# Optimization experiments

Measured on AMD Instinct MI355X. Metric: run time of the kernel, lower is better.

The kernel has to match this reference:

```python
import jax, jax.numpy as jnp
import numpy as np

N_NODES = 100000
N_EDGES = 1600000
D = 128
LEAKY_SLOPE = 0.01  # torch nn.LeakyReLU default


def setup_inputs() -> dict:
    key = jax.random.key(0)
    k1, k2, k3, k4 = jax.random.split(key, 4)
    in_states = jax.random.normal(k1, (N_NODES, D), dtype=jnp.float32)
    edges = jax.random.randint(k2, (2, N_EDGES), 0, N_NODES, dtype=jnp.int64)
    # Linear weights, kaiming-uniform-ish scale
    W_msg = jax.random.normal(k3, (D, D), dtype=jnp.float32) / np.sqrt(D)
    attn_w = jax.random.normal(k4, (2 * D,), dtype=jnp.float32) / np.sqrt(2 * D)
    W_res = jnp.eye(D, dtype=jnp.float32)  # eye-initialized, frozen residual proj
    passthrough_coef = jnp.ones((1,), dtype=jnp.float32)
    return {"in_states": in_states, "edges": edges, "W_msg": W_msg,
            "attn_w": attn_w, "W_res": W_res, "passthrough_coef": passthrough_coef}


def reference(in_states, edges, W_msg, attn_w, W_res, passthrough_coef):
    n_nodes = in_states.shape[0]
    src, dst = edges[0], edges[1]

    # message transform (dropout in eval mode -> identity)
    messages = in_states @ W_msg.T                       # [N, D]

    # attention score: Linear(2D->1) on cat([m_from, m_to]) == split dot products
    s_from = messages @ attn_w[:D]                       # [N]
    s_to = messages @ attn_w[D:]                         # [N]
    e = s_from[src] + s_to[dst]                          # [E]
    e = jnp.where(e >= 0, e, LEAKY_SLOPE * e)            # LeakyReLU

    # indexed (segment) softmax over destination nodes
    seg_max = jax.ops.segment_max(e, dst, num_segments=n_nodes)
    e_exp = jnp.exp(e - seg_max[dst])
    seg_sum = jax.ops.segment_sum(e_exp, dst, num_segments=n_nodes)
    alpha = e_exp / seg_sum[dst]                         # [E]

    # weighted scatter-add aggregation
    scaled = alpha[:, None] * messages[src]              # [E, D]
    merged = jax.ops.segment_sum(scaled, dst, num_segments=n_nodes)  # [N, D]

    new_states_res = jax.nn.relu(merged)
    old_passthrough = (in_states @ W_res.T) * jax.nn.sigmoid(passthrough_coef[0])
    return old_passthrough + new_states_res
```

## Files before the change

kernel.cpp:

```cpp
#include <hip/hip_runtime.h>
#include <hip/hip_fp16.h>


#define DD 128
#define NPB 32
#define LEAKY 0.01f
#define BSH 3
#define BSZ 8

#define FMA4(A, XS, W)                                        \
  A.x = fmaf((XS), (W).x, A.x); A.y = fmaf((XS), (W).y, A.y); \
  A.z = fmaf((XS), (W).z, A.z); A.w = fmaf((XS), (W).w, A.w)

__global__ void k_init(const int* __restrict__ e, const float* __restrict__ Wr,
                       int* __restrict__ flag, int* __restrict__ bcnt, int nb) {
  const int b = blockIdx.x;
  if (b == 0) {
    if (threadIdx.x == 0) {
      int all0 = 1;
      for (int i = 0; i < 64; ++i)
        if (e[2 * i + 1] != 0) { all0 = 0; break; }
      flag[0] = all0;
    }
  } else if (b == 1) {
    __shared__ int ok_s;
    if (threadIdx.x == 0) ok_s = 1;
    __syncthreads();
    int ok = 1;
    for (int i = threadIdx.x; i < DD * DD; i += 256) {
      float expect = ((i >> 7) == (i & (DD - 1))) ? 1.f : 0.f;
      if (Wr[i] != expect) ok = 0;
    }
    if (!ok) ok_s = 0;
    __syncthreads();
    if (threadIdx.x == 0) flag[1] = ok_s;
  } else {
    int i = (b - 2) * 256 + threadIdx.x;
    if (i < nb) bcnt[i] = 0;
  }
}

__global__ void k_prep(const float* __restrict__ Wm, const float* __restrict__ Wr,
                       float* __restrict__ WTm, float* __restrict__ WTr,
                       const int* __restrict__ edges, int n_edges, int n_nodes,
                       const int* __restrict__ flag, int* __restrict__ bcnt) {
  const int b = blockIdx.x;
  if (b < 64) {
    int idx = b * 256 + threadIdx.x;
    int j = idx >> 7, k = idx & (DD - 1);
    WTm[k * DD + j] = Wm[idx];
    WTr[k * DD + j] = Wr[idx];
  } else {
    int i = (b - 64) * 256 + threadIdx.x;
    if (i < n_edges) {
      int d = flag[0] ? ((const int2*)edges)[n_edges + i].x : edges[n_edges + i];
      if ((unsigned)d < (unsigned)n_nodes) atomicAdd(&bcnt[d >> BSH], 1);
    }
  }
}

__global__ __launch_bounds__(256) void k_scan_a(const int* __restrict__ cnt, int n,
                                                int* __restrict__ outp,
                                                int* __restrict__ bsum) {
  __shared__ int lds[256];
  const int t = threadIdx.x;
  const int base = blockIdx.x * 1024 + t * 4;
  int v0 = 0, v1 = 0, v2 = 0, v3 = 0;
  if (base + 3 < n) {
    int4 q = *(const int4*)(cnt + base);
    v0 = q.x; v1 = q.y; v2 = q.z; v3 = q.w;
  } else {
    if (base + 0 < n) v0 = cnt[base + 0];
    if (base + 1 < n) v1 = cnt[base + 1];
    if (base + 2 < n) v2 = cnt[base + 2];
    if (base + 3 < n) v3 = cnt[base + 3];
  }
  const int tsum = v0 + v1 + v2 + v3;
  int val = tsum;
  lds[t] = val;
  __syncthreads();
  for (int off = 1; off < 256; off <<= 1) {
    int a = (t >= off) ? lds[t - off] : 0;
    __syncthreads();
    val += a;
    lds[t] = val;
    __syncthreads();
  }
  int o0 = val - tsum;
  int o1 = o0 + v0, o2 = o1 + v1, o3 = o2 + v2;
  if (base + 0 < n) outp[base + 0] = o0;
  if (base + 1 < n) outp[base + 1] = o1;
  if (base + 2 < n) outp[base + 2] = o2;
  if (base + 3 < n) outp[base + 3] = o3;
  if (t == 255) bsum[blockIdx.x] = val;
}

__global__ void k_scan_b(int* __restrict__ bsum, int nbk,
                         int* __restrict__ bstart, int nb) {
  __shared__ int lds[256];
  const int t = threadIdx.x;
  int v = (t < nbk) ? bsum[t] : 0;
  int val = v;
  lds[t] = val;
  __syncthreads();
  for (int off = 1; off < 256; off <<= 1) {
    int a = (t >= off) ? lds[t - off] : 0;
    __syncthreads();
    val += a;
    lds[t] = val;
    __syncthreads();
  }
  if (t < nbk) bsum[t] = val - v;
  if (t == nbk - 1) bstart[nb] = val;
}

__global__ void k_scan_c(int* __restrict__ bstart, int* __restrict__ bcursor,
                         const int* __restrict__ bsum, int nb) {
  const int off = bsum[blockIdx.x];
  const int base = blockIdx.x * 1024 + threadIdx.x * 4;
#pragma unroll
  for (int c = 0; c < 4; ++c) {
    int idx = base + c;
    if (idx < nb) {
      int r = bstart[idx] + off;
      bstart[idx] = r;
      bcursor[idx] = r;
    }
  }
}

__global__ __launch_bounds__(256) void k_mscat(
    const float* __restrict__ x, const float* __restrict__ WTm,
    const float* __restrict__ WTr, const float* __restrict__ attn_w,
    const float* __restrict__ coef, const int* __restrict__ flag, int n_nodes,
    __half* __restrict__ mh, float* __restrict__ s_from,
    float* __restrict__ s_to, float* __restrict__ out, int msg_blocks,
    const int* __restrict__ edges, int n_edges, int* __restrict__ bcursor,
    int* __restrict__ packed) {
  __shared__ float4 lw4[32 * 32];
  __shared__ float4 lx4[NPB * 32];
  __shared__ float lds_aw[2 * DD];
  const int t = threadIdx.x;

  if ((int)blockIdx.x >= msg_blocks) {
    int i = (blockIdx.x - msg_blocks) * 256 + t;
    if (i < n_edges) {
      int d, s;
      if (flag[0]) {
        d = ((const int2*)edges)[n_edges + i].x;
        s = ((const int2*)edges)[i].x;
      } else {
        d = edges[n_edges + i];
        s = edges[i];
      }
      if ((unsigned)d < (unsigned)n_nodes) {
        if ((unsigned)s >= (unsigned)n_nodes) s = 0;
        int pos = atomicAdd(&bcursor[d >> BSH], 1);
        packed[pos] = (s << BSH) | (d & (BSZ - 1));
      }
    }
    return;
  }

  const int base = blockIdx.x * NPB;
  const int nvalid = min(NPB, n_nodes - base);

  const float4* xs = (const float4*)(x + (size_t)base * DD);
  const int nflt4 = nvalid * 32;
  for (int i = t; i < nflt4; i += 256) lx4[i] = xs[i];
  if (t < 2 * DD) lds_aw[t] = attn_w[t];

  const int j4 = t & 31;
  const int g = t >> 5;
  const int r0 = (g * 4 + 0) * 32, r1 = r0 + 32, r2 = r1 + 32, r3 = r2 + 32;

  float4 a0, a1, a2, a3;

#define GEMM128(WT)                                                           \
  a0 = a1 = a2 = a3 = make_float4(0.f, 0.f, 0.f, 0.f);                        \
  _Pragma("unroll 1")                                                         \
  for (int chunk = 0; chunk < 4; ++chunk) {                                   \
    __syncthreads();                                                          \
    const float4* wsrc = (const float4*)((WT) + chunk * 32 * DD);             \
    lw4[t] = wsrc[t];                                                         \
    lw4[t + 256] = wsrc[t + 256];                                             \
    lw4[t + 512] = wsrc[t + 512];                                             \
    lw4[t + 768] = wsrc[t + 768];                                             \
    __syncthreads();                                                          \
    const int xb = chunk * 8;                                                 \
    _Pragma("unroll 2")                                                       \
    for (int k = 0; k < 32; k += 4) {                                         \
      float4 w0 = lw4[(k + 0) * 32 + j4];                                     \
      float4 w1 = lw4[(k + 1) * 32 + j4];                                     \
      float4 w2 = lw4[(k + 2) * 32 + j4];                                     \
      float4 w3 = lw4[(k + 3) * 32 + j4];                                     \
      float4 x0 = lx4[r0 + xb + (k >> 2)];                                    \
      float4 x1 = lx4[r1 + xb + (k >> 2)];                                    \
      float4 x2 = lx4[r2 + xb + (k >> 2)];                                    \
      float4 x3 = lx4[r3 + xb + (k >> 2)];                                    \
      FMA4(a0, x0.x, w0); FMA4(a0, x0.y, w1);                                 \
      FMA4(a0, x0.z, w2); FMA4(a0, x0.w, w3);                                 \
      FMA4(a1, x1.x, w0); FMA4(a1, x1.y, w1);                                 \
      FMA4(a1, x1.z, w2); FMA4(a1, x1.w, w3);                                 \
      FMA4(a2, x2.x, w0); FMA4(a2, x2.y, w1);                                 \
      FMA4(a2, x2.z, w2); FMA4(a2, x2.w, w3);                                 \
      FMA4(a3, x3.x, w0); FMA4(a3, x3.y, w1);                                 \
      FMA4(a3, x3.z, w2); FMA4(a3, x3.w, w3);                                 \
    }                                                                         \
  }

  GEMM128(WTm);
  {
    float4 av[4] = {a0, a1, a2, a3};
#pragma unroll
    for (int b = 0; b < 4; ++b) {
      int n = g * 4 + b;
      if (n < nvalid) {
        int gn = base + n;
        float4 v = av[b];
        union { __half2 h2[2]; uint2 u; } pk;
        pk.h2[0] = __floats2half2_rn(v.x, v.y);
        pk.h2[1] = __floats2half2_rn(v.z, v.w);
        ((uint2*)(mh + (size_t)gn * DD))[j4] = pk.u;
        float sf = v.x * lds_aw[4 * j4] + v.y * lds_aw[4 * j4 + 1] +
                   v.z * lds_aw[4 * j4 + 2] + v.w * lds_aw[4 * j4 + 3];
        float stv = v.x * lds_aw[DD + 4 * j4] + v.y * lds_aw[DD + 4 * j4 + 1] +
                    v.z * lds_aw[DD + 4 * j4 + 2] + v.w * lds_aw[DD + 4 * j4 + 3];
#pragma unroll
        for (int m = 16; m; m >>= 1) {
          sf += __shfl_xor(sf, m, 32);
          stv += __shfl_xor(stv, m, 32);
        }
        if (j4 == 0) { s_from[gn] = sf; s_to[gn] = stv; }
      }
    }
  }

  const float sig = 1.f / (1.f + __expf(-coef[0]));
  if (flag[1]) {
    float4* od = (float4*)(out + (size_t)base * DD);
    for (int i = t; i < nflt4; i += 256) {
      float4 v = lx4[i];
      v.x *= sig; v.y *= sig; v.z *= sig; v.w *= sig;
      od[i] = v;
    }
  } else {
    GEMM128(WTr);
    float4 av[4] = {a0, a1, a2, a3};
#pragma unroll
    for (int b = 0; b < 4; ++b) {
      int n = g * 4 + b;
      if (n < nvalid) {
        int gn = base + n;
        float4 v = av[b];
        v.x *= sig; v.y *= sig; v.z *= sig; v.w *= sig;
        ((float4*)(out + (size_t)gn * DD))[j4] = v;
      }
    }
  }
#undef GEMM128
}

__global__ __launch_bounds__(256) void k_bsort(
    const int* __restrict__ bstart, const int* __restrict__ packed,
    int nb, int n_nodes, int n_edges_total,
    int* __restrict__ srcs, int* __restrict__ row_start) {
  const int lane = threadIdx.x & 63;
  const int b = blockIdx.x * 4 + (threadIdx.x >> 6);
  if (b >= nb) return;
  const int start = bstart[b], end = bstart[b + 1];
  const int nbase = b << BSH;
  if (b == 0 && lane == 0) row_start[n_nodes] = n_edges_total;

  int c0 = 0, c1 = 0, c2 = 0, c3 = 0, c4 = 0, c5 = 0, c6 = 0, c7 = 0;
  for (int cb = start; cb < end; cb += 64) {
    const bool act = (cb + lane) < end;
    const int u = act ? packed[cb + lane] : 0;
    const int dl = u & (BSZ - 1);
    const unsigned long long b0 = __ballot(act && (dl & 1));
    const unsigned long long b1 = __ballot(act && (dl & 2));
    const unsigned long long b2 = __ballot(act && (dl & 4));
    const unsigned long long ba = __ballot(act);
    c0 += __popcll(~b0 & ~b1 & ~b2 & ba);
    c1 += __popcll( b0 & ~b1 & ~b2 & ba);
    c2 += __popcll(~b0 &  b1 & ~b2 & ba);
    c3 += __popcll( b0 &  b1 & ~b2 & ba);
    c4 += __popcll(~b0 & ~b1 &  b2 & ba);
    c5 += __popcll( b0 & ~b1 &  b2 & ba);
    c6 += __popcll(~b0 &  b1 &  b2 & ba);
    c7 += __popcll( b0 &  b1 &  b2 & ba);
  }
  const int o0 = 0, o1 = o0 + c0, o2 = o1 + c1, o3 = o2 + c2, o4 = o3 + c3,
            o5 = o4 + c4, o6 = o5 + c5, o7 = o6 + c6;
  if (lane == 0) {
    if (nbase + 0 < n_nodes) row_start[nbase + 0] = start + o0;
    if (nbase + 1 < n_nodes) row_start[nbase + 1] = start + o1;
    if (nbase + 2 < n_nodes) row_start[nbase + 2] = start + o2;
    if (nbase + 3 < n_nodes) row_start[nbase + 3] = start + o3;
    if (nbase + 4 < n_nodes) row_start[nbase + 4] = start + o4;
    if (nbase + 5 < n_nodes) row_start[nbase + 5] = start + o5;
    if (nbase + 6 < n_nodes) row_start[nbase + 6] = start + o6;
    if (nbase + 7 < n_nodes) row_start[nbase + 7] = start + o7;
  }
  int r0 = o0, r1 = o1, r2 = o2, r3 = o3, r4 = o4, r5 = o5, r6 = o6, r7 = o7;
  for (int cb = start; cb < end; cb += 64) {
    const bool act = (cb + lane) < end;
    const int u = act ? packed[cb + lane] : 0;
    const int dl = u & (BSZ - 1);
    const unsigned long long b0 = __ballot(act && (dl & 1));
    const unsigned long long b1 = __ballot(act && (dl & 2));
    const unsigned long long b2 = __ballot(act && (dl & 4));
    const unsigned long long ba = __ballot(act);
    const unsigned long long m0 = (dl & 1) ? b0 : ~b0;
    const unsigned long long m1 = (dl & 2) ? b1 : ~b1;
    const unsigned long long m2 = (dl & 4) ? b2 : ~b2;
    const unsigned long long mymask = m0 & m1 & m2 & ba;
    const int rank = __popcll(mymask & ((1ull << lane) - 1ull));
    int basep = r0;
    basep = (dl == 1) ? r1 : basep;
    basep = (dl == 2) ? r2 : basep;
    basep = (dl == 3) ? r3 : basep;
    basep = (dl == 4) ? r4 : basep;
    basep = (dl == 5) ? r5 : basep;
    basep = (dl == 6) ? r6 : basep;
    basep = (dl == 7) ? r7 : basep;
    if (act) srcs[start + basep + rank] = u >> BSH;
    r0 += __popcll(~b0 & ~b1 & ~b2 & ba);
    r1 += __popcll( b0 & ~b1 & ~b2 & ba);
    r2 += __popcll(~b0 &  b1 & ~b2 & ba);
    r3 += __popcll( b0 &  b1 & ~b2 & ba);
    r4 += __popcll(~b0 & ~b1 &  b2 & ba);
    r5 += __popcll( b0 & ~b1 &  b2 & ba);
    r6 += __popcll(~b0 &  b1 &  b2 & ba);
    r7 += __popcll( b0 &  b1 &  b2 & ba);
  }
}

__global__ __launch_bounds__(256) void k_nagg(
    const int* __restrict__ row_start, const int* __restrict__ srcs,
    const float* __restrict__ s_from, const float* __restrict__ s_to,
    const __half* __restrict__ mh, int n_nodes, float* __restrict__ out) {
  const int lane = threadIdx.x & 63;
  const int v = blockIdx.x * 4 + (threadIdx.x >> 6);
  if (v >= n_nodes) return;
  const int start = row_start[v];
  const int end = row_start[v + 1];
  if (start >= end) return;
  const float st = s_to[v];

  float wsum = 0.f;
  float ax = 0.f, ay = 0.f;
  for (int cbase = start; cbase < end; cbase += 64) {
    const int cnt = min(64, end - cbase);
    int s = 0;
    float w = 0.f;
    if (lane < cnt) {
      s = srcs[cbase + lane];
      float xx = s_from[s] + st;
      xx = (xx >= 0.f) ? xx : LEAKY * xx;
      w = __expf(xx);
    }
    wsum += w;
#pragma unroll 8
    for (int i = 0; i < cnt; ++i) {
      int si = __shfl(s, i, 64);
      float wi = __shfl(w, i, 64);
      const float2 mf =
          __half22float2(((const __half2*)(mh + (size_t)si * DD))[lane]);
      ax = fmaf(wi, mf.x, ax);
      ay = fmaf(wi, mf.y, ay);
    }
  }
#pragma unroll
  for (int m = 32; m; m >>= 1) wsum += __shfl_xor(wsum, m, 64);
  const float inv = 1.f / wsum;
  ax *= inv; ay *= inv;
  ax = (ax > 0.f) ? ax : 0.f;
  ay = (ay > 0.f) ? ay : 0.f;
  float2* orow = (float2*)(out + (size_t)v * DD);
  float2 po = orow[lane];
  orow[lane] = make_float2(po.x + ax, po.y + ay);
}

extern "C" void kernel_launch(void* const* d_in, const int* in_sizes, int n_in,
                              void* d_out, int out_size, void* d_ws, size_t ws_size,
                              hipStream_t stream) {
  const float* x = (const float*)d_in[0];
  const int* edges = (const int*)d_in[1];
  const float* Wm = (const float*)d_in[2];
  const float* aw = (const float*)d_in[3];
  const float* Wr = (const float*)d_in[4];
  const float* coef = (const float*)d_in[5];
  float* out = (float*)d_out;

  const int N = in_sizes[0] / DD;
  const int E = in_sizes[1] / 2;
  const int nb = (N + BSZ - 1) / BSZ;

  const size_t need = ((size_t)N * DD * 2 + 256)
                    + 2 * ((size_t)N * 4 + 256)
                    + 2 * ((size_t)DD * DD * 4 + 256)
                    + 3 * ((size_t)(nb + 1) * 4 + 512)
                    + ((size_t)(N + 1) * 4 + 256)
                    + 2048
                    + 2 * ((size_t)E * 4 + 256);
  if (ws_size < need) return;

  char* w = (char*)d_ws;
  auto alloc = [&](size_t bytes) {
    char* p = w;
    w += (bytes + 255) & ~(size_t)255;
    return p;
  };
  __half* mh     = (__half*)alloc((size_t)N * DD * 2);
  float* s_from  = (float*)alloc((size_t)N * 4);
  float* s_to    = (float*)alloc((size_t)N * 4);
  float* WTm     = (float*)alloc((size_t)DD * DD * 4);
  float* WTr     = (float*)alloc((size_t)DD * DD * 4);
  int*   bcnt    = (int*)alloc((size_t)nb * 4);
  int*   bstart  = (int*)alloc((size_t)(nb + 1) * 4);
  int*   bcursor = (int*)alloc((size_t)nb * 4);
  int*   row_start = (int*)alloc((size_t)(N + 1) * 4);
  int*   flag    = (int*)alloc(256);
  int*   bsum    = (int*)alloc(256 * 4);
  int*   packed  = (int*)alloc((size_t)E * 4);
  int*   srcs    = (int*)alloc((size_t)E * 4);

  const int MB = (N + NPB - 1) / NPB;
  const int EB = (E + 255) / 256;
  const int ZB = (nb + 255) / 256;
  const int SB = (nb + 1023) / 1024;

  k_init<<<2 + ZB, 256, 0, stream>>>(edges, Wr, flag, bcnt, nb);
  k_prep<<<64 + EB, 256, 0, stream>>>(Wm, Wr, WTm, WTr, edges, E, N, flag, bcnt);
  k_scan_a<<<SB, 256, 0, stream>>>(bcnt, nb, bstart, bsum);
  k_scan_b<<<1, 256, 0, stream>>>(bsum, SB, bstart, nb);
  k_scan_c<<<SB, 256, 0, stream>>>(bstart, bcursor, bsum, nb);
  k_mscat<<<MB + EB, 256, 0, stream>>>(x, WTm, WTr, aw, coef, flag, N,
                                       mh, s_from, s_to, out, MB,
                                       edges, E, bcursor, packed);
  k_bsort<<<(nb + 3) / 4, 256, 0, stream>>>(bstart, packed, nb, N, E,
                                            srcs, row_start);
  k_nagg<<<(N + 3) / 4, 256, 0, stream>>>(row_start, srcs, s_from, s_to,
                                          mh, N, out);
}
```

Before: 445.8 us.

## Compute message GEMM with split-fp16 MFMA instead of scalar FP32 FMAs

Replaces the LDS-tiled scalar FP32 GEMM in k_mscat with MFMA 16x16x32 f16 instructions. Both activations and weights are split into high and low fp16 parts, and three MFMA products are summed to recover near-FP32 accuracy. The weights are pre-swizzled into the MFMA operand layout in k_prep, and the attention score reductions are reworked to fit the MFMA output layout. This is meant to cut the FP32 ALU cost of the 100k x 128 x 128 GEMM, at the price of some precision loss and scattered 2-byte stores of mh.

```diff
diff --git a/kernel.cpp b/kernel.cpp
--- a/kernel.cpp
+++ b/kernel.cpp
@@ -8,9 +8,8 @@
 #define BSH 3
 #define BSZ 8
 
-#define FMA4(A, XS, W)                                        \
-  A.x = fmaf((XS), (W).x, A.x); A.y = fmaf((XS), (W).y, A.y); \
-  A.z = fmaf((XS), (W).z, A.z); A.w = fmaf((XS), (W).w, A.w)
+typedef _Float16 f16x8 __attribute__((ext_vector_type(8)));
+typedef float f32x4 __attribute__((ext_vector_type(4)));
 
 __global__ void k_init(const int* __restrict__ e, const float* __restrict__ Wr,
                        int* __restrict__ flag, int* __restrict__ bcnt, int nb) {
@@ -41,15 +40,24 @@
 }
 
 __global__ void k_prep(const float* __restrict__ Wm, const float* __restrict__ Wr,
-                       float* __restrict__ WTm, float* __restrict__ WTr,
+                       __half* __restrict__ Bmh, __half* __restrict__ Bml,
+                       __half* __restrict__ Brh, __half* __restrict__ Brl,
                        const int* __restrict__ edges, int n_edges, int n_nodes,
                        const int* __restrict__ flag, int* __restrict__ bcnt) {
   const int b = blockIdx.x;
   if (b < 64) {
-    int idx = b * 256 + threadIdx.x;
-    int j = idx >> 7, k = idx & (DD - 1);
-    WTm[k * DD + j] = Wm[idx];
-    WTr[k * DD + j] = Wr[idx];
+    int i = b * 256 + threadIdx.x;
+    int j = i & 7, l = (i >> 3) & 63, c = (i >> 9) & 3, ct = i >> 11;
+    int k = 32 * c + 8 * (l >> 4) + j;
+    int col = 16 * ct + (l & 15);
+    float wm = Wm[col * DD + k];
+    __half h = __float2half(wm);
+    Bmh[i] = h;
+    Bml[i] = __float2half(wm - __half2float(h));
+    float wr = Wr[col * DD + k];
+    __half h2 = __float2half(wr);
+    Brh[i] = h2;
+    Brl[i] = __float2half(wr - __half2float(h2));
   } else {
     int i = (b - 64) * 256 + threadIdx.x;
     if (i < n_edges) {
@@ -130,16 +138,18 @@
 }
 
 __global__ __launch_bounds__(256) void k_mscat(
-    const float* __restrict__ x, const float* __restrict__ WTm,
-    const float* __restrict__ WTr, const float* __restrict__ attn_w,
+    const float* __restrict__ x, const __half* __restrict__ Bmh,
+    const __half* __restrict__ Bml, const __half* __restrict__ Brh,
+    const __half* __restrict__ Brl, const float* __restrict__ attn_w,
     const float* __restrict__ coef, const int* __restrict__ flag, int n_nodes,
     __half* __restrict__ mh, float* __restrict__ s_from,
     float* __restrict__ s_to, float* __restrict__ out, int msg_blocks,
     const int* __restrict__ edges, int n_edges, int* __restrict__ bcursor,
     int* __restrict__ packed) {
-  __shared__ float4 lw4[32 * 32];
-  __shared__ float4 lx4[NPB * 32];
+  __shared__ __half Ah[2 * 4 * 64 * 8];
+  __shared__ __half Al[2 * 4 * 64 * 8];
   __shared__ float lds_aw[2 * DD];
+  __shared__ float sc[2][NPB][2];
   const int t = threadIdx.x;
 
   if ((int)blockIdx.x >= msg_blocks) {
@@ -162,103 +172,153 @@
     return;
   }
 
-  const int base = blockIdx.x * NPB;
-  const int nvalid = min(NPB, n_nodes - base);
-
-  const float4* xs = (const float4*)(x + (size_t)base * DD);
-  const int nflt4 = nvalid * 32;
-  for (int i = t; i < nflt4; i += 256) lx4[i] = xs[i];
-  if (t < 2 * DD) lds_aw[t] = attn_w[t];
-
-  const int j4 = t & 31;
-  const int g = t >> 5;
-  const int r0 = (g * 4 + 0) * 32, r1 = r0 + 32, r2 = r1 + 32, r3 = r2 + 32;
-
-  float4 a0, a1, a2, a3;
-
-#define GEMM128(WT)                                                           \
-  a0 = a1 = a2 = a3 = make_float4(0.f, 0.f, 0.f, 0.f);                        \
-  _Pragma("unroll 1")                                                         \
-  for (int chunk = 0; chunk < 4; ++chunk) {                                   \
-    __syncthreads();                                                          \
-    const float4* wsrc = (const float4*)((WT) + chunk * 32 * DD);             \
-    lw4[t] = wsrc[t];                                                         \
-    lw4[t + 256] = wsrc[t + 256];                                             \
-    lw4[t + 512] = wsrc[t + 512];                                             \
-    lw4[t + 768] = wsrc[t + 768];                                             \
-    __syncthreads();                                                          \
-    const int xb = chunk * 8;                                                 \
-    _Pragma("unroll 2")                                                       \
-    for (int k = 0; k < 32; k += 4) {                                         \
-      float4 w0 = lw4[(k + 0) * 32 + j4];                                     \
-      float4 w1 = lw4[(k + 1) * 32 + j4];                                     \
-      float4 w2 = lw4[(k + 2) * 32 + j4];                                     \
-      float4 w3 = lw4[(k + 3) * 32 + j4];                                     \
-      float4 x0 = lx4[r0 + xb + (k >> 2)];                                    \
-      float4 x1 = lx4[r1 + xb + (k >> 2)];                                    \
-      float4 x2 = lx4[r2 + xb + (k >> 2)];                                    \
-      float4 x3 = lx4[r3 + xb + (k >> 2)];                                    \
-      FMA4(a0, x0.x, w0); FMA4(a0, x0.y, w1);                                 \
-      FMA4(a0, x0.z, w2); FMA4(a0, x0.w, w3);                                 \
-      FMA4(a1, x1.x, w0); FMA4(a1, x1.y, w1);                                 \
-      FMA4(a1, x1.z, w2); FMA4(a1, x1.w, w3);                                 \
-      FMA4(a2, x2.x, w0); FMA4(a2, x2.y, w1);                                 \
-      FMA4(a2, x2.z, w2); FMA4(a2, x2.w, w3);                                 \
-      FMA4(a3, x3.x, w0); FMA4(a3, x3.y, w1);                                 \
-      FMA4(a3, x3.z, w2); FMA4(a3, x3.w, w3);                                 \
-    }                                                                         \
-  }
-
-  GEMM128(WTm);
+  const int nb0 = blockIdx.x * NPB;
+  const int nvalid = min(NPB, n_nodes - nb0);
+
+  const float4* xs = (const float4*)(x + (size_t)nb0 * DD);
+#pragma unroll
+  for (int i = 0; i < 4; ++i) {
+    int f4 = t + i * 256;
+    int n = f4 >> 5, q = f4 & 31;
+    int c = q >> 3, hi = (q & 7) >> 1, j0 = (q & 1) * 4;
+    int nt2 = n >> 4, row = n & 15;
+    int l2 = row | (hi << 4);
+    int h0 = ((nt2 * 4 + c) * 64 + l2) * 8 + j0;
+    float4 v = (n < nvalid) ? xs[f4] : make_float4(0.f, 0.f, 0.f, 0.f);
+    __half hx = __float2half(v.x), hy = __float2half(v.y),
+           hz = __float2half(v.z), hw = __float2half(v.w);
+    union { __half2 h2[2]; uint2 u; } ph, pl;
+    ph.h2[0] = __halves2half2(hx, hy);
+    ph.h2[1] = __halves2half2(hz, hw);
+    pl.h2[0] = __halves2half2(__float2half(v.x - __half2float(hx)),
+                              __float2half(v.y - __half2float(hy)));
+    pl.h2[1] = __halves2half2(__float2half(v.z - __half2float(hz)),
+                              __float2half(v.w - __half2float(hw)));
+    ((uint2*)Ah)[h0 >> 2] = ph.u;
+    ((uint2*)Al)[h0 >> 2] = pl.u;
+  }
+  lds_aw[t] = attn_w[t];
+  __syncthreads();
+
+  const int l = t & 63;
+  const int wv = t >> 6;
+  const int nt = wv & 1;
+  const int ch = wv >> 1;
+
+  f32x4 acc[4] = {{0,0,0,0},{0,0,0,0},{0,0,0,0},{0,0,0,0}};
   {
-    float4 av[4] = {a0, a1, a2, a3};
-#pragma unroll
-    for (int b = 0; b < 4; ++b) {
-      int n = g * 4 + b;
-      if (n < nvalid) {
-        int gn = base + n;
-        float4 v = av[b];
-        union { __half2 h2[2]; uint2 u; } pk;
-        pk.h2[0] = __floats2half2_rn(v.x, v.y);
-        pk.h2[1] = __floats2half2_rn(v.z, v.w);
-        ((uint2*)(mh + (size_t)gn * DD))[j4] = pk.u;
-        float sf = v.x * lds_aw[4 * j4] + v.y * lds_aw[4 * j4 + 1] +
-                   v.z * lds_aw[4 * j4 + 2] + v.w * lds_aw[4 * j4 + 3];
-        float stv = v.x * lds_aw[DD + 4 * j4] + v.y * lds_aw[DD + 4 * j4 + 1] +
-                    v.z * lds_aw[DD + 4 * j4 + 2] + v.w * lds_aw[DD + 4 * j4 + 3];
-#pragma unroll
-        for (int m = 16; m; m >>= 1) {
-          sf += __shfl_xor(sf, m, 32);
-          stv += __shfl_xor(stv, m, 32);
-        }
-        if (j4 == 0) { s_from[gn] = sf; s_to[gn] = stv; }
+    const f16x8* BH = (const f16x8*)Bmh;
+    const f16x8* BL = (const f16x8*)Bml;
+#pragma unroll
+    for (int c = 0; c < 4; ++c) {
+      f16x8 ah = *(const f16x8*)(Ah + ((nt * 4 + c) * 64 + l) * 8);
+      f16x8 al = *(const f16x8*)(Al + ((nt * 4 + c) * 64 + l) * 8);
+#pragma unroll
+      for (int ci = 0; ci < 4; ++ci) {
+        int ct = ch * 4 + ci;
+        f16x8 bh = BH[(ct * 4 + c) * 64 + l];
+        f16x8 bl = BL[(ct * 4 + c) * 64 + l];
+        acc[ci] = __builtin_amdgcn_mfma_f32_16x16x32_f16(ah, bh, acc[ci], 0, 0, 0);
+        acc[ci] = __builtin_amdgcn_mfma_f32_16x16x32_f16(ah, bl, acc[ci], 0, 0, 0);
+        acc[ci] = __builtin_amdgcn_mfma_f32_16x16x32_f16(al, bh, acc[ci], 0, 0, 0);
       }
+    }
+  }
+
+#pragma unroll
+  for (int ci = 0; ci < 4; ++ci) {
+#pragma unroll
+    for (int r = 0; r < 4; ++r) {
+      int node = nb0 + 16 * nt + (l >> 4) * 4 + r;
+      int col = 64 * ch + 16 * ci + (l & 15);
+      if (node < n_nodes) mh[(size_t)node * DD + col] = __float2half(acc[ci][r]);
+    }
+  }
+#pragma unroll
+  for (int r = 0; r < 4; ++r) {
+    float pf = 0.f, pt = 0.f;
+#pragma unroll
+    for (int ci = 0; ci < 4; ++ci) {
+      int col = 64 * ch + 16 * ci + (l & 15);
+      float m = acc[ci][r];
+      pf = fmaf(m, lds_aw[col], pf);
+      pt = fmaf(m, lds_aw[DD + col], pt);
+    }
+#pragma unroll
+    for (int msk = 1; msk < 16; msk <<= 1) {
+      pf += __shfl_xor(pf, msk, 64);
+      pt += __shfl_xor(pt, msk, 64);
+    }
+    if ((l & 15) == 0) {
+      int li = 16 * nt + (l >> 4) * 4 + r;
+      sc[ch][li][0] = pf;
+      sc[ch][li][1] = pt;
+    }
+  }
+  __syncthreads();
+  if (t < NPB) {
+    int node = nb0 + t;
+    if (node < n_nodes) {
+      s_from[node] = sc[0][t][0] + sc[1][t][0];
+      s_to[node]   = sc[0][t][1] + sc[1][t][1];
     }
   }
 
   const float sig = 1.f / (1.f + __expf(-coef[0]));
   if (flag[1]) {
-    float4* od = (float4*)(out + (size_t)base * DD);
-    for (int i = t; i < nflt4; i += 256) {
-      float4 v = lx4[i];
-      v.x *= sig; v.y *= sig; v.z *= sig; v.w *= sig;
-      od[i] = v;
+    float4* od = (float4*)(out + (size_t)nb0 * DD);
+#pragma unroll
+    for (int i = 0; i < 4; ++i) {
+      int f4 = t + i * 256;
+      int n = f4 >> 5, q = f4 & 31;
+      if (n < nvalid) {
+        int c = q >> 3, hi = (q & 7) >> 1, j0 = (q & 1) * 4;
+        int nt2 = n >> 4, row = n & 15;
+        int l2 = row | (hi << 4);
+        int h0 = ((nt2 * 4 + c) * 64 + l2) * 8 + j0;
+        union { __half2 h2[2]; uint2 u; } ph, pl;
+        ph.u = ((const uint2*)Ah)[h0 >> 2];
+        pl.u = ((const uint2*)Al)[h0 >> 2];
+        float2 a0 = __half22float2(ph.h2[0]);
+        float2 a1 = __half22float2(ph.h2[1]);
+        float2 b0 = __half22float2(pl.h2[0]);
+        float2 b1 = __half22float2(pl.h2[1]);
+        float4 v;
+        v.x = sig * (a0.x + b0.x);
+        v.y = sig * (a0.y + b0.y);
+        v.z = sig * (a1.x + b1.x);
+        v.w = sig * (a1.y + b1.y);
+        od[f4] = v;
+      }
     }
   } else {
-    GEMM128(WTr);
-    float4 av[4] = {a0, a1, a2, a3};
-#pragma unroll
-    for (int b = 0; b < 4; ++b) {
-      int n = g * 4 + b;
-      if (n < nvalid) {
-        int gn = base + n;
-        float4 v = av[b];
-        v.x *= sig; v.y *= sig; v.z *= sig; v.w *= sig;
-        ((float4*)(out + (size_t)gn * DD))[j4] = v;
+    f32x4 acr[4] = {{0,0,0,0},{0,0,0,0},{0,0,0,0},{0,0,0,0}};
+    const f16x8* BH = (const f16x8*)Brh;
+    const f16x8* BL = (const f16x8*)Brl;
+#pragma unroll
+    for (int c = 0; c < 4; ++c) {
+      f16x8 ah = *(const f16x8*)(Ah + ((nt * 4 + c) * 64 + l) * 8);
+      f16x8 al = *(const f16x8*)(Al + ((nt * 4 + c) * 64 + l) * 8);
+#pragma unroll
+      for (int ci = 0; ci < 4; ++ci) {
+        int ct = ch * 4 + ci;
+        f16x8 bh = BH[(ct * 4 + c) * 64 + l];
+        f16x8 bl = BL[(ct * 4 + c) * 64 + l];
+        acr[ci] = __builtin_amdgcn_mfma_f32_16x16x32_f16(ah, bh, acr[ci], 0, 0, 0);
+        acr[ci] = __builtin_amdgcn_mfma_f32_16x16x32_f16(ah, bl, acr[ci], 0, 0, 0);
+        acr[ci] = __builtin_amdgcn_mfma_f32_16x16x32_f16(al, bh, acr[ci], 0, 0, 0);
       }
     }
-  }
-#undef GEMM128
+#pragma unroll
+    for (int ci = 0; ci < 4; ++ci) {
+#pragma unroll
+      for (int r = 0; r < 4; ++r) {
+        int node = nb0 + 16 * nt + (l >> 4) * 4 + r;
+        int col = 64 * ch + 16 * ci + (l & 15);
+        if (node < n_nodes) out[(size_t)node * DD + col] = sig * acr[ci][r];
+      }
+    }
+  }
 }
 
 __global__ __launch_bounds__(256) void k_bsort(
@@ -399,7 +459,7 @@
 
   const size_t need = ((size_t)N * DD * 2 + 256)
                     + 2 * ((size_t)N * 4 + 256)
-                    + 2 * ((size_t)DD * DD * 4 + 256)
+                    + 4 * ((size_t)DD * DD * 2 + 256)
                     + 3 * ((size_t)(nb + 1) * 4 + 512)
                     + ((size_t)(N + 1) * 4 + 256)
                     + 2048
@@ -415,8 +475,10 @@
   __half* mh     = (__half*)alloc((size_t)N * DD * 2);
   float* s_from  = (float*)alloc((size_t)N * 4);
   float* s_to    = (float*)alloc((size_t)N * 4);
-  float* WTm     = (float*)alloc((size_t)DD * DD * 4);
-  float* WTr     = (float*)alloc((size_t)DD * DD * 4);
+  __half* Bmh    = (__half*)alloc((size_t)DD * DD * 2);
+  __half* Bml    = (__half*)alloc((size_t)DD * DD * 2);
+  __half* Brh    = (__half*)alloc((size_t)DD * DD * 2);
+  __half* Brl    = (__half*)alloc((size_t)DD * DD * 2);
   int*   bcnt    = (int*)alloc((size_t)nb * 4);
   int*   bstart  = (int*)alloc((size_t)(nb + 1) * 4);
   int*   bcursor = (int*)alloc((size_t)nb * 4);
@@ -432,11 +494,12 @@
   const int SB = (nb + 1023) / 1024;
 
   k_init<<<2 + ZB, 256, 0, stream>>>(edges, Wr, flag, bcnt, nb);
-  k_prep<<<64 + EB, 256, 0, stream>>>(Wm, Wr, WTm, WTr, edges, E, N, flag, bcnt);
+  k_prep<<<64 + EB, 256, 0, stream>>>(Wm, Wr, Bmh, Bml, Brh, Brl,
+                                      edges, E, N, flag, bcnt);
   k_scan_a<<<SB, 256, 0, stream>>>(bcnt, nb, bstart, bsum);
   k_scan_b<<<1, 256, 0, stream>>>(bsum, SB, bstart, nb);
   k_scan_c<<<SB, 256, 0, stream>>>(bstart, bcursor, bsum, nb);
-  k_mscat<<<MB + EB, 256, 0, stream>>>(x, WTm, WTr, aw, coef, flag, N,
+  k_mscat<<<MB + EB, 256, 0, stream>>>(x, Bmh, Bml, Brh, Brl, aw, coef, flag, N,
                                        mh, s_from, s_to, out, MB,
                                        edges, E, bcursor, packed);
   k_bsort<<<(nb + 3) / 4, 256, 0, stream>>>(bstart, packed, nb, N, E,
```

New measurement: 447.0 us. Within noise of the previous version (+0.3%).
